# Kernel tuning notes

Measured on AMD Instinct MI355X. Metric: run time of the kernel, lower is better.

Reference implementation:

```python
import jax, jax.numpy as jnp
import numpy as np

N = 1_000_000
NUM_CLASSES = 100
N_BINS = 15


def setup_inputs() -> dict:
    key = jax.random.key(0)
    k1, k2 = jax.random.split(key)
    logits = jax.random.normal(k1, (N, NUM_CLASSES), dtype=jnp.float32)
    labels = jax.random.randint(k2, (N,), 0, NUM_CLASSES, dtype=jnp.int64)
    return {"logits": logits, "labels": labels, "n_bins": N_BINS}


def reference(logits, labels, n_bins):
    # softmax -> per-sample confidence (max prob) and prediction (argmax)
    softmaxes = jax.nn.softmax(logits, axis=1)
    confidences = jnp.max(softmaxes, axis=1)
    predictions = jnp.argmax(softmaxes, axis=1).astype(jnp.int32)
    accuracies = (predictions == labels.astype(jnp.int32)).astype(confidences.dtype)

    num_classes = logits.shape[1]
    num_data = logits.shape[0]

    # Bin assignment matching (lower, upper] intervals of linspace(0,1,n_bins+1):
    # conf in ((b)/n_bins, (b+1)/n_bins] -> bin b. conf > 0 always (softmax max).
    bin_idx = jnp.clip(
        jnp.ceil(confidences * n_bins).astype(jnp.int32) - 1, 0, n_bins - 1
    )
    # Fused cell id over (predicted class, bin)
    cell = predictions * n_bins + bin_idx  # [N]
    num_cells = num_classes * n_bins

    sum_conf = jax.ops.segment_sum(confidences, cell, num_segments=num_cells)
    sum_acc = jax.ops.segment_sum(accuracies, cell, num_segments=num_cells)

    # Per non-empty cell: |mean_conf - mean_acc| * count/N = |sum_conf - sum_acc|/N;
    # empty cells contribute exactly 0.
    ece = jnp.sum(jnp.abs(sum_conf - sum_acc)) / num_data
    return ece
```

## Files before the change

### kernel.cpp

```cpp
#include <hip/hip_runtime.h>
#include <math.h>


constexpr int C  = 100;
constexpr int NB = 15;
constexpr int NCELLS = C * NB;
constexpr int RPB  = 8;
constexpr int F4R  = 25;
constexpr int F4S  = 27;
constexpr int SLOTS = RPB * F4S;
constexpr int WAVES = 4;
constexpr int GRID_MAIN = 1024;

__global__ void ece_zero(float* __restrict__ ws, int n) {
    int i = blockIdx.x * blockDim.x + threadIdx.x;
    if (i < n) ws[i] = 0.0f;
}

__device__ __forceinline__ void load_lds_16B(const void* gsrc, void* ldst) {
    __builtin_amdgcn_global_load_lds(
        (const __attribute__((address_space(1))) void*)gsrc,
        (__attribute__((address_space(3))) void*)ldst, 16, 0, 0);
}

__global__ __launch_bounds__(256)
void ece_main(const float* __restrict__ logits,
              const int* __restrict__ labels,
              int nchunk, float* __restrict__ cellsums) {
    __shared__ float4 stage[WAVES][2][SLOTS];
    __shared__ float  hist[2 * NCELLS];

    for (int i = threadIdx.x; i < 2 * NCELLS; i += blockDim.x) hist[i] = 0.0f;
    __syncthreads();

    const int wid   = threadIdx.x >> 6;
    const int lane  = threadIdx.x & 63;
    const int gwave = blockIdx.x * WAVES + wid;
    const int gstr  = gridDim.x * WAVES;
    const float4* logits4 = reinterpret_cast<const float4*>(logits);
    constexpr float LOG2E = 1.4426950408889634f;

    int offs[4];
    #pragma unroll
    for (int i = 0; i < 4; ++i) {
        int s = i * 64 + lane;
        int r = s / F4S, c = s - r * F4S;
        if (c > F4R - 1) c = F4R - 1;
        if (s >= SLOTS) { r = 0; c = 0; }
        offs[i] = r * F4R + c;
    }
    const bool act3 = lane < (SLOTS - 192);

    float4* buf0 = &stage[wid][0][0];
    float4* buf1 = &stage[wid][1][0];

    const int o = lane >> 3;
    const int j = lane & 7;

#define DO_STAGE(BUF, CHUNK, LABDST)                                          \
    {                                                                         \
        const float4* src_ = logits4 + (size_t)(CHUNK) * (RPB * F4R);         \
        LABDST = labels[(CHUNK) * RPB + o];                                   \
        char* lb_ = (char*)(BUF);                                             \
        load_lds_16B(src_ + offs[0], lb_);                                    \
        load_lds_16B(src_ + offs[1], lb_ + 64 * 16);                          \
        load_lds_16B(src_ + offs[2], lb_ + 128 * 16);                         \
        if (act3) load_lds_16B(src_ + offs[3], lb_ + 192 * 16);               \
    }

    int lab_cur = 0, lab_nxt = 0;
    int k = gwave;
    int cur = 0;
    if (k < nchunk) DO_STAGE(buf0, k, lab_cur);

    for (; k < nchunk; k += gstr) {
        const int kn = k + gstr;
        if (kn < nchunk) {
            DO_STAGE(cur ? buf1 : buf0 + SLOTS , 0, lab_nxt);
        }
        (void)0;
        break;
    }
#undef DO_STAGE

    {
        float4* bufs[2] = { buf0, buf1 };
        lab_cur = 0; lab_nxt = 0; cur = 0;
        k = gwave;
        if (k < nchunk) {
            const float4* src = logits4 + (size_t)k * (RPB * F4R);
            lab_cur = labels[k * RPB + o];
            char* lb = (char*)bufs[0];
            load_lds_16B(src + offs[0], lb);
            load_lds_16B(src + offs[1], lb + 64 * 16);
            load_lds_16B(src + offs[2], lb + 128 * 16);
            if (act3) load_lds_16B(src + offs[3], lb + 192 * 16);
        }

        for (; k < nchunk; k += gstr) {
            const int kn = k + gstr;
            if (kn < nchunk) {
                const float4* src = logits4 + (size_t)kn * (RPB * F4R);
                lab_nxt = labels[kn * RPB + o];
                char* lb = (char*)bufs[cur ^ 1];
                load_lds_16B(src + offs[0], lb);
                load_lds_16B(src + offs[1], lb + 64 * 16);
                load_lds_16B(src + offs[2], lb + 128 * 16);
                if (act3) load_lds_16B(src + offs[3], lb + 192 * 16);
                asm volatile("s_waitcnt vmcnt(5)" ::: "memory");
            } else {
                asm volatile("s_waitcnt vmcnt(0)" ::: "memory");
            }
            __builtin_amdgcn_sched_barrier(0);

            const float4* rp = bufs[cur] + o * F4S;
            float4 v0 = rp[j], v1 = rp[j + 8], v2 = rp[j + 16];
            float4 v3;
            const bool tail = (j == 0);
            if (tail) v3 = rp[24];

            float m = v0.x; int am = 4 * j;
            if (v0.y > m) { m = v0.y; am = 4 * j + 1; }
            if (v0.z > m) { m = v0.z; am = 4 * j + 2; }
            if (v0.w > m) { m = v0.w; am = 4 * j + 3; }
            if (v1.x > m) { m = v1.x; am = 32 + 4 * j; }
            if (v1.y > m) { m = v1.y; am = 32 + 4 * j + 1; }
            if (v1.z > m) { m = v1.z; am = 32 + 4 * j + 2; }
            if (v1.w > m) { m = v1.w; am = 32 + 4 * j + 3; }
            if (v2.x > m) { m = v2.x; am = 64 + 4 * j; }
            if (v2.y > m) { m = v2.y; am = 64 + 4 * j + 1; }
            if (v2.z > m) { m = v2.z; am = 64 + 4 * j + 2; }
            if (v2.w > m) { m = v2.w; am = 64 + 4 * j + 3; }
            if (tail) {
                if (v3.x > m) { m = v3.x; am = 96; }
                if (v3.y > m) { m = v3.y; am = 97; }
                if (v3.z > m) { m = v3.z; am = 98; }
                if (v3.w > m) { m = v3.w; am = 99; }
            }
            #pragma unroll
            for (int off = 1; off < 8; off <<= 1) {
                float om  = __shfl_xor(m, off, 64);
                int   oam = __shfl_xor(am, off, 64);
                if (om > m || (om == m && oam < am)) { m = om; am = oam; }
            }

            const float ml = m * LOG2E;
            float s = exp2f(__fmaf_rn(v0.x, LOG2E, -ml))
                    + exp2f(__fmaf_rn(v0.y, LOG2E, -ml))
                    + exp2f(__fmaf_rn(v0.z, LOG2E, -ml))
                    + exp2f(__fmaf_rn(v0.w, LOG2E, -ml));
            s += exp2f(__fmaf_rn(v1.x, LOG2E, -ml))
               + exp2f(__fmaf_rn(v1.y, LOG2E, -ml))
               + exp2f(__fmaf_rn(v1.z, LOG2E, -ml))
               + exp2f(__fmaf_rn(v1.w, LOG2E, -ml));
            s += exp2f(__fmaf_rn(v2.x, LOG2E, -ml))
               + exp2f(__fmaf_rn(v2.y, LOG2E, -ml))
               + exp2f(__fmaf_rn(v2.z, LOG2E, -ml))
               + exp2f(__fmaf_rn(v2.w, LOG2E, -ml));
            if (tail) {
                s += exp2f(__fmaf_rn(v3.x, LOG2E, -ml))
                   + exp2f(__fmaf_rn(v3.y, LOG2E, -ml))
                   + exp2f(__fmaf_rn(v3.z, LOG2E, -ml))
                   + exp2f(__fmaf_rn(v3.w, LOG2E, -ml));
            }
            #pragma unroll
            for (int off = 1; off < 8; off <<= 1) s += __shfl_xor(s, off, 64);

            if (tail) {
                float conf = 1.0f / s;
                int b = (int)ceilf(conf * (float)NB) - 1;
                b = b < 0 ? 0 : (b > NB - 1 ? NB - 1 : b);
                int cell = am * NB + b;
                atomicAdd(&hist[cell], conf);
                if (lab_cur == am) atomicAdd(&hist[NCELLS + cell], 1.0f);
            }

            asm volatile("s_waitcnt lgkmcnt(0)" ::: "memory");
            lab_cur = lab_nxt;
            cur ^= 1;
        }
    }

    __syncthreads();
    for (int i = threadIdx.x; i < 2 * NCELLS; i += blockDim.x) {
        float v = hist[i];
        if (v != 0.0f) atomicAdd(&cellsums[i], v);
    }
}

__global__ void ece_final(const float* __restrict__ cellsums,
                          float invN, float* __restrict__ out) {
    __shared__ float red[256];
    float t = 0.0f;
    for (int i = threadIdx.x; i < NCELLS; i += blockDim.x)
        t += fabsf(cellsums[i] - cellsums[NCELLS + i]);
    red[threadIdx.x] = t;
    __syncthreads();
    for (int w = 128; w > 0; w >>= 1) {
        if (threadIdx.x < w) red[threadIdx.x] += red[threadIdx.x + w];
        __syncthreads();
    }
    if (threadIdx.x == 0) out[0] = red[0] * invN;
}

extern "C" void kernel_launch(void* const* d_in, const int* in_sizes, int n_in,
                              void* d_out, int out_size, void* d_ws, size_t ws_size,
                              hipStream_t stream) {
    const float* logits = (const float*)d_in[0];
    const int*   labels = (const int*)d_in[1];

    const int N = in_sizes[1];
    const int nchunk = N / RPB;

    float* cellsums = (float*)d_ws;
    float* out = (float*)d_out;

    {
        int n = 2 * NCELLS;
        ece_zero<<<(n + 255) / 256, 256, 0, stream>>>(cellsums, n);
    }

    ece_main<<<GRID_MAIN, 256, 0, stream>>>(logits, labels, nchunk, cellsums);

    ece_final<<<1, 256, 0, stream>>>(cellsums, 1.0f / (float)N, out);
}
```

Baseline: 100.6 us.

## Replace per-wave double-buffered staging with block-wide single-buffer tiles and nontemporal loads

Moves from per-wave 8-row chunks with double-buffered async LDS loads and manual waitcnt to a block-wide 32-row tile that is loaded into one LDS buffer and bracketed by __syncthreads. The grid grows from 1024 to 1536 blocks and the loads carry a nontemporal cache hint. This simplifies the code and relies on occupancy across blocks to hide latency instead of explicit in-wave prefetch. The risk is that two block barriers per tile and the lack of overlap inside a block expose memory latency.

```diff
diff --git a/kernel.cpp b/kernel.cpp
--- a/kernel.cpp
+++ b/kernel.cpp
@@ -5,184 +5,129 @@
 constexpr int C  = 100;
 constexpr int NB = 15;
 constexpr int NCELLS = C * NB;
-constexpr int RPB  = 8;
+constexpr int ROWS = 32;
 constexpr int F4R  = 25;
-constexpr int F4S  = 27;
-constexpr int SLOTS = RPB * F4S;
-constexpr int WAVES = 4;
-constexpr int GRID_MAIN = 1024;
+constexpr int STR  = 26;
+constexpr int TILE_F4 = ROWS * STR;
+constexpr int THREADS = 256;
+constexpr int GRID_MAIN = 1536;
 
 __global__ void ece_zero(float* __restrict__ ws, int n) {
     int i = blockIdx.x * blockDim.x + threadIdx.x;
     if (i < n) ws[i] = 0.0f;
 }
 
-__device__ __forceinline__ void load_lds_16B(const void* gsrc, void* ldst) {
+__device__ __forceinline__ void load_lds_16B_nt(const void* gsrc, void* ldst) {
     __builtin_amdgcn_global_load_lds(
         (const __attribute__((address_space(1))) void*)gsrc,
-        (__attribute__((address_space(3))) void*)ldst, 16, 0, 0);
+        (__attribute__((address_space(3))) void*)ldst, 16, 0, 2);
 }
 
-__global__ __launch_bounds__(256)
+__global__ __launch_bounds__(THREADS)
 void ece_main(const float* __restrict__ logits,
               const int* __restrict__ labels,
-              int nchunk, float* __restrict__ cellsums) {
-    __shared__ float4 stage[WAVES][2][SLOTS];
+              int ntiles, float* __restrict__ cellsums) {
+    __shared__ float4 stage[TILE_F4];
     __shared__ float  hist[2 * NCELLS];
 
-    for (int i = threadIdx.x; i < 2 * NCELLS; i += blockDim.x) hist[i] = 0.0f;
-    __syncthreads();
+    for (int i = threadIdx.x; i < 2 * NCELLS; i += THREADS) hist[i] = 0.0f;
 
-    const int wid   = threadIdx.x >> 6;
-    const int lane  = threadIdx.x & 63;
-    const int gwave = blockIdx.x * WAVES + wid;
-    const int gstr  = gridDim.x * WAVES;
+    const int tid = threadIdx.x;
+    const int o   = tid >> 3;
+    const int j   = tid & 7;
+    const int wbase = (tid >> 6) << 6;
+
+    int offs[4]; bool val[4];
+    #pragma unroll
+    for (int i = 0; i < 4; ++i) {
+        int s = i * 256 + tid;
+        int r = s / STR, c = s - r * STR;
+        val[i]  = (s < TILE_F4) && (c < F4R);
+        offs[i] = r * F4R + c;
+    }
+
     const float4* logits4 = reinterpret_cast<const float4*>(logits);
     constexpr float LOG2E = 1.4426950408889634f;
 
-    int offs[4];
-    #pragma unroll
-    for (int i = 0; i < 4; ++i) {
-        int s = i * 64 + lane;
-        int r = s / F4S, c = s - r * F4S;
-        if (c > F4R - 1) c = F4R - 1;
-        if (s >= SLOTS) { r = 0; c = 0; }
-        offs[i] = r * F4R + c;
-    }
-    const bool act3 = lane < (SLOTS - 192);
+    for (int tile = blockIdx.x; tile < ntiles; tile += gridDim.x) {
+        const int row0 = tile * ROWS;
+        const float4* tb = logits4 + (size_t)row0 * F4R;
 
-    float4* buf0 = &stage[wid][0][0];
-    float4* buf1 = &stage[wid][1][0];
+        #pragma unroll
+        for (int i = 0; i < 4; ++i) {
+            if (val[i]) load_lds_16B_nt(tb + offs[i], &stage[i * 256 + wbase]);
+        }
+        __syncthreads();
 
-    const int o = lane >> 3;
-    const int j = lane & 7;
+        const int row = row0 + o;
+        int lab = -1;
+        if (j == 0) lab = __builtin_nontemporal_load(&labels[row]);
 
-#define DO_STAGE(BUF, CHUNK, LABDST)                                          \
-    {                                                                         \
-        const float4* src_ = logits4 + (size_t)(CHUNK) * (RPB * F4R);         \
-        LABDST = labels[(CHUNK) * RPB + o];                                   \
-        char* lb_ = (char*)(BUF);                                             \
-        load_lds_16B(src_ + offs[0], lb_);                                    \
-        load_lds_16B(src_ + offs[1], lb_ + 64 * 16);                          \
-        load_lds_16B(src_ + offs[2], lb_ + 128 * 16);                         \
-        if (act3) load_lds_16B(src_ + offs[3], lb_ + 192 * 16);               \
+        const float4* rp = &stage[o * STR];
+        float4 v0 = rp[j], v1 = rp[j + 8], v2 = rp[j + 16];
+        float4 v3;
+        const bool tail = (j == 0);
+        if (tail) v3 = rp[24];
+
+        float m = v0.x; int am = 4 * j;
+        if (v0.y > m) { m = v0.y; am = 4 * j + 1; }
+        if (v0.z > m) { m = v0.z; am = 4 * j + 2; }
+        if (v0.w > m) { m = v0.w; am = 4 * j + 3; }
+        if (v1.x > m) { m = v1.x; am = 32 + 4 * j; }
+        if (v1.y > m) { m = v1.y; am = 32 + 4 * j + 1; }
+        if (v1.z > m) { m = v1.z; am = 32 + 4 * j + 2; }
+        if (v1.w > m) { m = v1.w; am = 32 + 4 * j + 3; }
+        if (v2.x > m) { m = v2.x; am = 64 + 4 * j; }
+        if (v2.y > m) { m = v2.y; am = 64 + 4 * j + 1; }
+        if (v2.z > m) { m = v2.z; am = 64 + 4 * j + 2; }
+        if (v2.w > m) { m = v2.w; am = 64 + 4 * j + 3; }
+        if (tail) {
+            if (v3.x > m) { m = v3.x; am = 96; }
+            if (v3.y > m) { m = v3.y; am = 97; }
+            if (v3.z > m) { m = v3.z; am = 98; }
+            if (v3.w > m) { m = v3.w; am = 99; }
+        }
+        #pragma unroll
+        for (int off = 1; off < 8; off <<= 1) {
+            float om  = __shfl_xor(m, off, 64);
+            int   oam = __shfl_xor(am, off, 64);
+            if (om > m || (om == m && oam < am)) { m = om; am = oam; }
+        }
+
+        const float ml = m * LOG2E;
+        float s = exp2f(__fmaf_rn(v0.x, LOG2E, -ml))
+                + exp2f(__fmaf_rn(v0.y, LOG2E, -ml))
+                + exp2f(__fmaf_rn(v0.z, LOG2E, -ml))
+                + exp2f(__fmaf_rn(v0.w, LOG2E, -ml));
+        s += exp2f(__fmaf_rn(v1.x, LOG2E, -ml))
+           + exp2f(__fmaf_rn(v1.y, LOG2E, -ml))
+           + exp2f(__fmaf_rn(v1.z, LOG2E, -ml))
+           + exp2f(__fmaf_rn(v1.w, LOG2E, -ml));
+        s += exp2f(__fmaf_rn(v2.x, LOG2E, -ml))
+           + exp2f(__fmaf_rn(v2.y, LOG2E, -ml))
+           + exp2f(__fmaf_rn(v2.z, LOG2E, -ml))
+           + exp2f(__fmaf_rn(v2.w, LOG2E, -ml));
+        if (tail) {
+            s += exp2f(__fmaf_rn(v3.x, LOG2E, -ml))
+               + exp2f(__fmaf_rn(v3.y, LOG2E, -ml))
+               + exp2f(__fmaf_rn(v3.z, LOG2E, -ml))
+               + exp2f(__fmaf_rn(v3.w, LOG2E, -ml));
+        }
+        #pragma unroll
+        for (int off = 1; off < 8; off <<= 1) s += __shfl_xor(s, off, 64);
+
+        if (j == 0) {
+            float conf = 1.0f / s;
+            int b = (int)ceilf(conf * (float)NB) - 1;
+            b = b < 0 ? 0 : (b > NB - 1 ? NB - 1 : b);
+            int cell = am * NB + b;
+            atomicAdd(&hist[cell], conf);
+            if (lab == am) atomicAdd(&hist[NCELLS + cell], 1.0f);
+        }
+        __syncthreads();
     }
 
-    int lab_cur = 0, lab_nxt = 0;
-    int k = gwave;
-    int cur = 0;
-    if (k < nchunk) DO_STAGE(buf0, k, lab_cur);
-
-    for (; k < nchunk; k += gstr) {
-        const int kn = k + gstr;
-        if (kn < nchunk) {
-            DO_STAGE(cur ? buf1 : buf0 + SLOTS , 0, lab_nxt);
-        }
-        (void)0;
-        break;
-    }
-#undef DO_STAGE
-
-    {
-        float4* bufs[2] = { buf0, buf1 };
-        lab_cur = 0; lab_nxt = 0; cur = 0;
-        k = gwave;
-        if (k < nchunk) {
-            const float4* src = logits4 + (size_t)k * (RPB * F4R);
-            lab_cur = labels[k * RPB + o];
-            char* lb = (char*)bufs[0];
-            load_lds_16B(src + offs[0], lb);
-            load_lds_16B(src + offs[1], lb + 64 * 16);
-            load_lds_16B(src + offs[2], lb + 128 * 16);
-            if (act3) load_lds_16B(src + offs[3], lb + 192 * 16);
-        }
-
-        for (; k < nchunk; k += gstr) {
-            const int kn = k + gstr;
-            if (kn < nchunk) {
-                const float4* src = logits4 + (size_t)kn * (RPB * F4R);
-                lab_nxt = labels[kn * RPB + o];
-                char* lb = (char*)bufs[cur ^ 1];
-                load_lds_16B(src + offs[0], lb);
-                load_lds_16B(src + offs[1], lb + 64 * 16);
-                load_lds_16B(src + offs[2], lb + 128 * 16);
-                if (act3) load_lds_16B(src + offs[3], lb + 192 * 16);
-                asm volatile("s_waitcnt vmcnt(5)" ::: "memory");
-            } else {
-                asm volatile("s_waitcnt vmcnt(0)" ::: "memory");
-            }
-            __builtin_amdgcn_sched_barrier(0);
-
-            const float4* rp = bufs[cur] + o * F4S;
-            float4 v0 = rp[j], v1 = rp[j + 8], v2 = rp[j + 16];
-            float4 v3;
-            const bool tail = (j == 0);
-            if (tail) v3 = rp[24];
-
-            float m = v0.x; int am = 4 * j;
-            if (v0.y > m) { m = v0.y; am = 4 * j + 1; }
-            if (v0.z > m) { m = v0.z; am = 4 * j + 2; }
-            if (v0.w > m) { m = v0.w; am = 4 * j + 3; }
-            if (v1.x > m) { m = v1.x; am = 32 + 4 * j; }
-            if (v1.y > m) { m = v1.y; am = 32 + 4 * j + 1; }
-            if (v1.z > m) { m = v1.z; am = 32 + 4 * j + 2; }
-            if (v1.w > m) { m = v1.w; am = 32 + 4 * j + 3; }
-            if (v2.x > m) { m = v2.x; am = 64 + 4 * j; }
-            if (v2.y > m) { m = v2.y; am = 64 + 4 * j + 1; }
-            if (v2.z > m) { m = v2.z; am = 64 + 4 * j + 2; }
-            if (v2.w > m) { m = v2.w; am = 64 + 4 * j + 3; }
-            if (tail) {
-                if (v3.x > m) { m = v3.x; am = 96; }
-                if (v3.y > m) { m = v3.y; am = 97; }
-                if (v3.z > m) { m = v3.z; am = 98; }
-                if (v3.w > m) { m = v3.w; am = 99; }
-            }
-            #pragma unroll
-            for (int off = 1; off < 8; off <<= 1) {
-                float om  = __shfl_xor(m, off, 64);
-                int   oam = __shfl_xor(am, off, 64);
-                if (om > m || (om == m && oam < am)) { m = om; am = oam; }
-            }
-
-            const float ml = m * LOG2E;
-            float s = exp2f(__fmaf_rn(v0.x, LOG2E, -ml))
-                    + exp2f(__fmaf_rn(v0.y, LOG2E, -ml))
-                    + exp2f(__fmaf_rn(v0.z, LOG2E, -ml))
-                    + exp2f(__fmaf_rn(v0.w, LOG2E, -ml));
-            s += exp2f(__fmaf_rn(v1.x, LOG2E, -ml))
-               + exp2f(__fmaf_rn(v1.y, LOG2E, -ml))
-               + exp2f(__fmaf_rn(v1.z, LOG2E, -ml))
-               + exp2f(__fmaf_rn(v1.w, LOG2E, -ml));
-            s += exp2f(__fmaf_rn(v2.x, LOG2E, -ml))
-               + exp2f(__fmaf_rn(v2.y, LOG2E, -ml))
-               + exp2f(__fmaf_rn(v2.z, LOG2E, -ml))
-               + exp2f(__fmaf_rn(v2.w, LOG2E, -ml));
-            if (tail) {
-                s += exp2f(__fmaf_rn(v3.x, LOG2E, -ml))
-                   + exp2f(__fmaf_rn(v3.y, LOG2E, -ml))
-                   + exp2f(__fmaf_rn(v3.z, LOG2E, -ml))
-                   + exp2f(__fmaf_rn(v3.w, LOG2E, -ml));
-            }
-            #pragma unroll
-            for (int off = 1; off < 8; off <<= 1) s += __shfl_xor(s, off, 64);
-
-            if (tail) {
-                float conf = 1.0f / s;
-                int b = (int)ceilf(conf * (float)NB) - 1;
-                b = b < 0 ? 0 : (b > NB - 1 ? NB - 1 : b);
-                int cell = am * NB + b;
-                atomicAdd(&hist[cell], conf);
-                if (lab_cur == am) atomicAdd(&hist[NCELLS + cell], 1.0f);
-            }
-
-            asm volatile("s_waitcnt lgkmcnt(0)" ::: "memory");
-            lab_cur = lab_nxt;
-            cur ^= 1;
-        }
-    }
-
-    __syncthreads();
-    for (int i = threadIdx.x; i < 2 * NCELLS; i += blockDim.x) {
+    for (int i = threadIdx.x; i < 2 * NCELLS; i += THREADS) {
         float v = hist[i];
         if (v != 0.0f) atomicAdd(&cellsums[i], v);
     }
@@ -210,7 +155,7 @@
     const int*   labels = (const int*)d_in[1];
 
     const int N = in_sizes[1];
-    const int nchunk = N / RPB;
+    const int ntiles = N / ROWS;
 
     float* cellsums = (float*)d_ws;
     float* out = (float*)d_out;
@@ -220,7 +165,7 @@
         ece_zero<<<(n + 255) / 256, 256, 0, stream>>>(cellsums, n);
     }
 
-    ece_main<<<GRID_MAIN, 256, 0, stream>>>(logits, labels, nchunk, cellsums);
+    ece_main<<<GRID_MAIN, THREADS, 0, stream>>>(logits, labels, ntiles, cellsums);
 
     ece_final<<<1, 256, 0, stream>>>(cellsums, 1.0f / (float)N, out);
 }
```

Result: slower. 112.4 us (+11.8%).
